# Kernel optimization log

Measured on AMD Instinct MI355X. Metric: run time of the kernel, lower is better.

The kernel has to match this reference:

```python
import jax, jax.numpy as jnp
import numpy as np

BS, NA, NE_, NL = 128, 3, 3, 3
NALL = NA - 1                 # n_allies
ENT = NA + NE_ + NL           # 9 entities
EM1 = ENT - 1                 # 8
HID = 64                      # hidden_dim
HEAD = 4
HIN = 9                       # hyper input dim
HYP = 64                      # hyper hidden dim
NRBF, RUB = 3, 10.0
EPS = 1e-7


def _lin_init(k, fan_in, fan_out):
    k1, k2 = jax.random.split(k)
    lim = 1.0 / np.sqrt(fan_in)
    w = jax.random.uniform(k1, (fan_in, fan_out), minval=-lim, maxval=lim, dtype=jnp.float32)
    b = jax.random.uniform(k2, (fan_out,), minval=-lim, maxval=lim, dtype=jnp.float32)
    return w, b


def setup_inputs():
    key = jax.random.key(0)
    ks = jax.random.split(key, 12)
    d = {}
    obs_dim = 4 + 2 * (NL + NALL + NE_) + 2 * (NALL + NE_)  # 30
    d["inputs"] = jax.random.normal(ks[0], (BS * NA, obs_dim), dtype=jnp.float32)
    d["hidden_state"] = jnp.zeros((1, HID), dtype=jnp.float32)
    d["actions"] = jax.random.normal(ks[1], (BS * NA, 2), dtype=jnp.float32)
    out_dim = (HIN + 1) * HID * HEAD  # 2560
    d["hA1_w"], d["hA1_b"] = _lin_init(ks[2], HIN, HYP)
    d["hA2_w"], d["hA2_b"] = _lin_init(ks[3], HYP, out_dim)
    d["hE1_w"], d["hE1_b"] = _lin_init(ks[4], HIN, HYP)
    d["hE2_w"], d["hE2_b"] = _lin_init(ks[5], HYP, out_dim)
    d["hL1_w"], d["hL1_b"] = _lin_init(ks[6], HIN, HYP)
    d["hL2_w"], d["hL2_b"] = _lin_init(ks[7], HYP, out_dim)
    d["merger_w"] = jnp.ones((1, HEAD, HID), dtype=jnp.float32)
    d["fc1_w"], d["fc1_b"] = _lin_init(ks[8], HID + 3, HID)
    d["fc2_w"], d["fc2_b"] = _lin_init(ks[9], HID, 1)
    return d


def _pair_out(feat, w1, b1, w2, b2):
    # hypernetwork: Linear(9,64) -> LeakyReLU -> Linear(64, (9+1)*64*4)
    h = jax.nn.leaky_relu(feat @ w1 + b1, negative_slope=0.01)
    out = h @ w2 + b2                               # (bs,NA,EM1,EM1,2560)
    nw = HIN * HID * HEAD
    w = out[..., :nw].reshape(feat.shape[:-1] + (HIN, HID * HEAD))
    b = out[..., nw:]
    y = jnp.einsum('...k,...kd->...d', feat, w) + b  # tiny 1x9 @ 9x256 per pair
    return y.reshape(feat.shape[:-1] + (HEAD, HID))


def _forward(inputs, actions, hA1_w, hA1_b, hA2_w, hA2_b, hE1_w, hE1_b, hE2_w, hE2_b,
             hL1_w, hL1_b, hL2_w, hL2_b, merger_w, fc1_w, fc1_b, fc2_w, fc2_b):
    bs = inputs.shape[0] // NA
    ob = inputs
    own = ob[:, :4].reshape(bs, NA, 4)
    i = 4
    lm_pos = ob[:, i:i + NL * 2].reshape(bs, NA, NL, 2); i += NL * 2
    ally_pos = ob[:, i:i + NALL * 2].reshape(bs, NA, NALL, 2); i += NALL * 2
    enemy_pos = ob[:, i:i + NE_ * 2].reshape(bs, NA, NE_, 2); i += NE_ * 2
    entity_pos = jnp.concatenate([ally_pos, enemy_pos, lm_pos], axis=-2)  # (bs,NA,EM1,2)
    ally_vel = ob[:, i:i + NALL * 2].reshape(bs, NA, NALL, 2); i += NALL * 2
    enemy_vel = ob[:, i:i + NE_ * 2].reshape(bs, NA, NE_, 2)
    lm_vel = jnp.zeros_like(lm_pos) - own[:, :, None, :2]
    entity_vel = jnp.concatenate([ally_vel, enemy_vel, lm_vel], axis=-2)  # (bs,NA,EM1,2)
    # rel_vel[b,a,j,i] = vel[i] - vel[j]
    rel_vel = entity_vel[:, :, None, :, :] - entity_vel[:, :, :, None, :]
    vel_norm = jnp.sqrt((entity_vel ** 2).sum(-1))
    sin_a = entity_vel[..., 1] / (vel_norm + EPS)
    cos_a = entity_vel[..., 0] / (vel_norm + EPS)
    act = actions.reshape(bs, NA, 2)
    act_norm = jnp.sqrt((act ** 2).sum(-1))        # (bs,NA)
    sin_b = act[..., 1] / (act_norm + EPS)
    cos_b = act[..., 0] / (act_norm + EPS)
    dist = jnp.sqrt((entity_pos ** 2).sum(-1))     # (bs,NA,EM1)
    sin_t = entity_pos[..., 1] / (dist + EPS)
    cos_t = entity_pos[..., 0] / (dist + EPS)
    # pair angles: A,C vary over last axis (i), B over second-to-last (j)
    sA, cA = sin_t[:, :, None, :], cos_t[:, :, None, :]
    sB, cB = sin_t[:, :, :, None], cos_t[:, :, :, None]
    sC, cC = sin_a[:, :, None, :], cos_a[:, :, None, :]
    angle_info = jnp.stack([sA * cB - cA * sB, cA * cB + sA * sB,
                            sC * cB - cC * sB, cC * cB + sC * sB], axis=-1)
    angle_info = jnp.broadcast_to(angle_info, (bs, NA, EM1, EM1, 4))
    sD, cD = sin_b[:, :, None], cos_b[:, :, None]
    act_angle = jnp.stack([sD * cos_t - cD * sin_t, cD * cos_t + sD * sin_t], axis=-1)  # (bs,NA,EM1,2)
    # gaussian RBF (schnet-style smearing, num_rbf=3, rbound_upper=10)
    offset = jnp.linspace(0.0, RUB, NRBF)
    coeff = -0.5 / (offset[1] - offset[0]) ** 2
    rbf = jnp.exp(coeff * (dist[..., None] - offset) ** 2)  # (bs,NA,EM1,NRBF)
    feat_dist = jnp.broadcast_to(rbf[:, :, None, :, :], (bs, NA, EM1, EM1, NRBF))
    feat = jnp.concatenate([feat_dist, angle_info, rel_vel], axis=-1)  # (bs,NA,EM1,EM1,9)
    ally_out = _pair_out(feat, hA1_w, hA1_b, hA2_w, hA2_b)
    enemy_out = _pair_out(feat, hE1_w, hE1_b, hE2_w, hE2_b)
    lm_out = _pair_out(feat, hL1_w, hL1_b, hL2_w, hL2_b)
    # type-based selection over the source-entity axis (dim 3), then sum-aggregate
    m = jnp.concatenate([ally_out[:, :, :, :NALL],
                         enemy_out[:, :, :, NALL:NALL + NE_],
                         lm_out[:, :, :, NALL + NE_:]], axis=3)
    m_sum = m.sum(axis=3)                               # (bs,NA,EM1,HEAD,HID)
    mw = jax.nn.softmax(merger_w, axis=1)               # (1,HEAD,HID)
    m_jki = (mw * m_sum).sum(axis=-2)                   # (bs,NA,EM1,HID)
    an = jnp.broadcast_to(act_norm[:, :, None], (bs, NA, EM1))[..., None]
    final = jnp.concatenate([m_jki, an, act_angle], axis=-1)  # (bs,NA,EM1,HID+3)
    x = jax.nn.relu(final)
    x = jax.nn.relu(x @ fc1_w + fc1_b)
    q = (x @ fc2_w + fc2_b).mean(axis=-2).reshape(-1, 1)  # (bs*NA,1)
    return q, x


def reference(inputs, hidden_state, actions, hA1_w, hA1_b, hA2_w, hA2_b,
              hE1_w, hE1_b, hE2_w, hE2_b, hL1_w, hL1_b, hL2_w, hL2_b,
              merger_w, fc1_w, fc1_b, fc2_w, fc2_b):
    q, x = _forward(inputs, actions, hA1_w, hA1_b, hA2_w, hA2_b,
                    hE1_w, hE1_b, hE2_w, hE2_b, hL1_w, hL1_b, hL2_w, hL2_b,
                    merger_w, fc1_w, fc1_b, fc2_w, fc2_b)
    return q, x
```

## Files before the change

### kernel.cpp

```cpp
#include <hip/hip_runtime.h>
#include <math.h>

#define EPS 1e-7f
#define ROWP 656
#define NETS 3
#define NROW_TOT (NETS*ROWP)
#define G4 (ROWP/4)
#define PERNET (ROWP*64)
#define PERNET4 (G4*64)

__global__ __launch_bounds__(256) void prep_w2r(
    const float* __restrict__ W2A, const float* __restrict__ b2A,
    const float* __restrict__ W2E, const float* __restrict__ b2E,
    const float* __restrict__ W2L, const float* __restrict__ b2L,
    const float* __restrict__ merger, float* __restrict__ W2r)
{
    int idx = blockIdx.x * 256 + threadIdx.x;
    if (idx >= NETS * PERNET4) return;
    int net = idx / PERNET4;
    int rem = idx - net * PERNET4;
    int g4  = rem >> 6;
    int hid = rem & 63;

    float m0 = merger[hid], m1 = merger[64+hid], m2 = merger[128+hid], m3 = merger[192+hid];
    float mx = fmaxf(fmaxf(m0, m1), fmaxf(m2, m3));
    float e0 = expf(m0-mx), e1 = expf(m1-mx), e2 = expf(m2-mx), e3 = expf(m3-mx);
    float inv = 1.0f / (e0+e1+e2+e3);
    float w0 = e0*inv, w1 = e1*inv, w2 = e2*inv, w3 = e3*inv;

    const float* W2 = (net==0) ? W2A : ((net==1) ? W2E : W2L);
    const float* b2 = (net==0) ? b2A : ((net==1) ? b2E : b2L);

    float4 v;
    float* vp = &v.x;
    #pragma unroll
    for (int r = 0; r < 4; ++r) {
        int row = g4*4 + r;
        float val = 0.0f;
        if (row < 650) {
            const float* src;
            int kk;
            if (row < 640) { int h = row / 10; kk = row - h*10; src = W2 + h*2560; }
            else           { kk = row - 640;                    src = b2; }
            int col = (kk < 9) ? kk*256 : 2304;
            val = w0*src[col+hid] + w1*src[col+64+hid] + w2*src[col+128+hid] + w3*src[col+192+hid];
        }
        vp[r] = val;
    }
    ((float4*)W2r)[idx] = v;
}

__global__ __launch_bounds__(256) void agent_kernel(
    const float* __restrict__ inputs, const float* __restrict__ actions,
    const float* __restrict__ W1A, const float* __restrict__ b1A,
    const float* __restrict__ W1E, const float* __restrict__ b1E,
    const float* __restrict__ W1L, const float* __restrict__ b1L,
    const float* __restrict__ W2r,
    const float* __restrict__ fc1w, const float* __restrict__ fc1b,
    const float* __restrict__ fc2w, const float* __restrict__ fc2b,
    float* __restrict__ out_q, float* __restrict__ out_x)
{
    __shared__ float sOb[32];
    __shared__ float sSt[8], sCt[8], sSa[8], sCa[8], sVx[8], sVy[8];
    __shared__ float sRbf[8][3];
    __shared__ float sAct[3];
    __shared__ float sF[64][10];
    __shared__ __align__(16) float sU[8 * NROW_TOT];
    __shared__ float sZp[4][8][64];
    __shared__ float sZ[8][64];
    __shared__ float sRed[4];

    const int tid   = threadIdx.x;
    const int agent = blockIdx.x;

    if (tid < 30) sOb[tid] = inputs[agent*30 + tid];
    if (tid == 30) sOb[30] = actions[agent*2 + 0];
    if (tid == 31) sOb[31] = actions[agent*2 + 1];
    __syncthreads();

    if (tid < 8) {
        int e = tid;
        float px, py, vx, vy;
        if (e < 2)      {           px = sOb[10+2*e]; py = sOb[11+2*e]; vx = sOb[20+2*e]; vy = sOb[21+2*e]; }
        else if (e < 5) { int t=e-2; px = sOb[14+2*t]; py = sOb[15+2*t]; vx = sOb[24+2*t]; vy = sOb[25+2*t]; }
        else            { int t=e-5; px = sOb[4+2*t];  py = sOb[5+2*t];  vx = -sOb[0];     vy = -sOb[1]; }
        float d  = sqrtf(px*px + py*py);
        sSt[e] = py / (d + EPS);
        sCt[e] = px / (d + EPS);
        float vn = sqrtf(vx*vx + vy*vy);
        sSa[e] = vy / (vn + EPS);
        sCa[e] = vx / (vn + EPS);
        sVx[e] = vx; sVy[e] = vy;
        sRbf[e][0] = expf(-0.02f * d * d);
        float d5  = d - 5.0f;  sRbf[e][1] = expf(-0.02f * d5  * d5);
        float d10 = d - 10.0f; sRbf[e][2] = expf(-0.02f * d10 * d10);
    }
    if (tid == 8) {
        float ax = sOb[30], ay = sOb[31];
        float an = sqrtf(ax*ax + ay*ay);
        sAct[0] = an;
        sAct[1] = ay / (an + EPS);
        sAct[2] = ax / (an + EPS);
    }
    __syncthreads();

    if (tid < 64) {
        int p = tid, j = p >> 3, k = p & 7;
        sF[p][0] = sRbf[k][0];
        sF[p][1] = sRbf[k][1];
        sF[p][2] = sRbf[k][2];
        sF[p][3] = sSt[k]*sCt[j] - sCt[k]*sSt[j];
        sF[p][4] = sCt[k]*sCt[j] + sSt[k]*sSt[j];
        sF[p][5] = sSa[k]*sCt[j] - sCa[k]*sSt[j];
        sF[p][6] = sCa[k]*sCt[j] + sSa[k]*sSt[j];
        sF[p][7] = sVx[k] - sVx[j];
        sF[p][8] = sVy[k] - sVy[j];
        sF[p][9] = 1.0f;
    }
    __syncthreads();

    for (int e = tid; e < 1920; e += 256) {
        if (e < 1536) {
            int j = e / 192, rem = e - j*192;
            int net = rem >> 6, h = rem & 63;
            int ks = (net==0) ? 0 : ((net==1) ? 2 : 5);
            int kn = (net==0) ? 2 : 3;
            const float* W1 = (net==0) ? W1A : ((net==1) ? W1E : W1L);
            const float* b1 = (net==0) ? b1A : ((net==1) ? b1E : b1L);
            float v[10];
            #pragma unroll
            for (int kk = 0; kk < 10; ++kk) v[kk] = 0.0f;
            for (int q = 0; q < kn; ++q) {
                int p = j*8 + ks + q;
                float acc = b1[h];
                #pragma unroll
                for (int kk = 0; kk < 9; ++kk) acc = fmaf(sF[p][kk], W1[kk*64 + h], acc);
                float H = (acc > 0.0f) ? acc : 0.01f*acc;
                #pragma unroll
                for (int kk = 0; kk < 10; ++kk) v[kk] = fmaf(H, sF[p][kk], v[kk]);
            }
            float* dst = sU + j*NROW_TOT + net*ROWP + h*10;
            #pragma unroll
            for (int kk = 0; kk < 10; ++kk) dst[kk] = v[kk];
        } else if (e < 1776) {
            int t = e - 1536;
            int j = t / 30, rem = t - j*30;
            int net = rem / 10, kk = rem - net*10;
            int ks = (net==0) ? 0 : ((net==1) ? 2 : 5);
            int kn = (net==0) ? 2 : 3;
            float v = 0.0f;
            for (int q = 0; q < kn; ++q) v += sF[j*8 + ks + q][kk];
            sU[j*NROW_TOT + net*ROWP + 640 + kk] = v;
        } else {
            int t = e - 1776;
            int j = t / 18, rem = t - j*18;
            int net = rem / 6, r = rem - net*6;
            sU[j*NROW_TOT + net*ROWP + 650 + r] = 0.0f;
        }
    }
    __syncthreads();

    {
        int lane = tid & 63, w = tid >> 6;
        float acc[8];
        #pragma unroll
        for (int j = 0; j < 8; ++j) acc[j] = 0.0f;
        const float4* Wp = (const float4*)W2r;
        for (int net = 0; net < NETS; ++net) {
            const float4* Wn = Wp + net*PERNET4;
            const float*  Ub = sU + net*ROWP;
            #pragma unroll 2
            for (int g = w; g < G4; g += 4) {
                float4 wv = Wn[g*64 + lane];
                int row = g*4;
                #pragma unroll
                for (int j = 0; j < 8; ++j) {
                    float4 u = *(const float4*)(Ub + j*NROW_TOT + row);
                    acc[j] = fmaf(u.x, wv.x, fmaf(u.y, wv.y, fmaf(u.z, wv.z, fmaf(u.w, wv.w, acc[j]))));
                }
            }
        }
        #pragma unroll
        for (int j = 0; j < 8; ++j) sZp[w][j][lane] = acc[j];
    }
    __syncthreads();
    for (int o = tid; o < 512; o += 256) {
        int j = o >> 6, c = o & 63;
        float z = sZp[0][j][c] + sZp[1][j][c] + sZp[2][j][c] + sZp[3][j][c];
        sZ[j][c] = (z > 0.0f) ? z : 0.0f;
    }
    __syncthreads();

    {
        float an  = sAct[0], sb = sAct[1], cb = sAct[2];
        float anr = (an > 0.0f) ? an : 0.0f;
        float myq = 0.0f;
        #pragma unroll
        for (int i = 0; i < 2; ++i) {
            int o = i*256 + tid;
            int j = o >> 6, c = o & 63;
            float acc = fc1b[c];
            #pragma unroll 8
            for (int d = 0; d < 64; ++d)
                acc = fmaf(sZ[j][d], fc1w[d*64 + c], acc);
            float aa0 = sb*sCt[j] - cb*sSt[j];
            float aa1 = cb*sCt[j] + sb*sSt[j];
            aa0 = (aa0 > 0.0f) ? aa0 : 0.0f;
            aa1 = (aa1 > 0.0f) ? aa1 : 0.0f;
            acc = fmaf(anr, fc1w[64*64 + c], acc);
            acc = fmaf(aa0, fc1w[65*64 + c], acc);
            acc = fmaf(aa1, fc1w[66*64 + c], acc);
            float x1 = (acc > 0.0f) ? acc : 0.0f;
            out_x[(agent*8 + j)*64 + c] = x1;
            myq = fmaf(x1, fc2w[c], myq);
        }
        for (int off = 32; off; off >>= 1) myq += __shfl_down(myq, off);
        int lane = tid & 63, w = tid >> 6;
        if (lane == 0) sRed[w] = myq;
        __syncthreads();
        if (tid == 0) out_q[agent] = (sRed[0] + sRed[1] + sRed[2] + sRed[3]) * 0.125f + fc2b[0];
    }
}

extern "C" void kernel_launch(void* const* d_in, const int* in_sizes, int n_in,
                              void* d_out, int out_size, void* d_ws, size_t ws_size,
                              hipStream_t stream) {
    const float* inputs  = (const float*)d_in[0];
    const float* actions = (const float*)d_in[2];
    const float* hA1_w = (const float*)d_in[3];  const float* hA1_b = (const float*)d_in[4];
    const float* hA2_w = (const float*)d_in[5];  const float* hA2_b = (const float*)d_in[6];
    const float* hE1_w = (const float*)d_in[7];  const float* hE1_b = (const float*)d_in[8];
    const float* hE2_w = (const float*)d_in[9];  const float* hE2_b = (const float*)d_in[10];
    const float* hL1_w = (const float*)d_in[11]; const float* hL1_b = (const float*)d_in[12];
    const float* hL2_w = (const float*)d_in[13]; const float* hL2_b = (const float*)d_in[14];
    const float* merger = (const float*)d_in[15];
    const float* fc1w = (const float*)d_in[16];  const float* fc1b = (const float*)d_in[17];
    const float* fc2w = (const float*)d_in[18];  const float* fc2b = (const float*)d_in[19];

    float* W2r = (float*)d_ws;
    float* q   = (float*)d_out;
    float* x   = q + 384;

    int total4 = NETS * PERNET4;
    prep_w2r<<<(total4 + 255)/256, 256, 0, stream>>>(hA2_w, hA2_b, hE2_w, hE2_b,
                                                     hL2_w, hL2_b, merger, W2r);
    agent_kernel<<<384, 256, 0, stream>>>(inputs, actions,
                                          hA1_w, hA1_b, hE1_w, hE1_b, hL1_w, hL1_b,
                                          W2r, fc1w, fc1b, fc2w, fc2b, q, x);
}
```

Measured before the change: 128.1 us.

## Reorder W2 rows k-major and register-tile the hyper GEMV over four hidden columns

The packed W2 rows are reordered to be k-major (row = kk*64 + h), and the sU staging is written to match. In the main reduction each lane now loads four weight float4s spanning 16-column strides and reuses each shared-memory U float4 across four outputs, with cross-quarter partial sums combined by xor shuffles. The aim is to cut LDS traffic per FMA and raise ILP, at the cost of more registers, which is why launch_bounds now requests a minimum of 2 blocks. A tail row-group is handled only by the q==0 lanes, and the 10-iteration split per wave assumes G4=164 divides into 4 waves of 41 groups.

```diff
diff --git a/kernel.cpp b/kernel.cpp
--- a/kernel.cpp
+++ b/kernel.cpp
@@ -6,7 +6,7 @@
 #define NETS 3
 #define NROW_TOT (NETS*ROWP)
 #define G4 (ROWP/4)
-#define PERNET (ROWP*64)
+#define GPW (G4/4)
 #define PERNET4 (G4*64)
 
 __global__ __launch_bounds__(256) void prep_w2r(
@@ -40,8 +40,8 @@
         if (row < 650) {
             const float* src;
             int kk;
-            if (row < 640) { int h = row / 10; kk = row - h*10; src = W2 + h*2560; }
-            else           { kk = row - 640;                    src = b2; }
+            if (row < 640) { kk = row >> 6; int h = row & 63; src = W2 + h*2560; }
+            else           { kk = row - 640;                  src = b2; }
             int col = (kk < 9) ? kk*256 : 2304;
             val = w0*src[col+hid] + w1*src[col+64+hid] + w2*src[col+128+hid] + w3*src[col+192+hid];
         }
@@ -50,7 +50,7 @@
     ((float4*)W2r)[idx] = v;
 }
 
-__global__ __launch_bounds__(256) void agent_kernel(
+__global__ __launch_bounds__(256, 2) void agent_kernel(
     const float* __restrict__ inputs, const float* __restrict__ actions,
     const float* __restrict__ W1A, const float* __restrict__ b1A,
     const float* __restrict__ W1E, const float* __restrict__ b1E,
@@ -139,9 +139,9 @@
                 #pragma unroll
                 for (int kk = 0; kk < 10; ++kk) v[kk] = fmaf(H, sF[p][kk], v[kk]);
             }
-            float* dst = sU + j*NROW_TOT + net*ROWP + h*10;
-            #pragma unroll
-            for (int kk = 0; kk < 10; ++kk) dst[kk] = v[kk];
+            float* dst = sU + j*NROW_TOT + net*ROWP + h;
+            #pragma unroll
+            for (int kk = 0; kk < 10; ++kk) dst[kk*64] = v[kk];
         } else if (e < 1776) {
             int t = e - 1536;
             int j = t / 30, rem = t - j*30;
@@ -161,27 +161,60 @@
     __syncthreads();
 
     {
-        int lane = tid & 63, w = tid >> 6;
-        float acc[8];
+        const int lane = tid & 63, w = tid >> 6;
+        const int q = lane >> 4, hh = lane & 15;
+        float acc[8][4];
         #pragma unroll
-        for (int j = 0; j < 8; ++j) acc[j] = 0.0f;
+        for (int j = 0; j < 8; ++j)
+            #pragma unroll
+            for (int k = 0; k < 4; ++k) acc[j][k] = 0.0f;
+
         const float4* Wp = (const float4*)W2r;
+        const int base = w * GPW;
         for (int net = 0; net < NETS; ++net) {
             const float4* Wn = Wp + net*PERNET4;
             const float*  Ub = sU + net*ROWP;
             #pragma unroll 2
-            for (int g = w; g < G4; g += 4) {
-                float4 wv = Wn[g*64 + lane];
-                int row = g*4;
+            for (int u = 0; u < 10; ++u) {
+                int g = base + u*4 + q;
+                const float4* wb = Wn + g*64 + hh;
+                float4 wk0 = wb[0], wk1 = wb[16], wk2 = wb[32], wk3 = wb[48];
+                float4 uj[8];
+                #pragma unroll
+                for (int j = 0; j < 8; ++j) uj[j] = *(const float4*)(Ub + j*NROW_TOT + g*4);
                 #pragma unroll
                 for (int j = 0; j < 8; ++j) {
-                    float4 u = *(const float4*)(Ub + j*NROW_TOT + row);
-                    acc[j] = fmaf(u.x, wv.x, fmaf(u.y, wv.y, fmaf(u.z, wv.z, fmaf(u.w, wv.w, acc[j]))));
+                    float4 uu = uj[j];
+                    acc[j][0] = fmaf(uu.x,wk0.x, fmaf(uu.y,wk0.y, fmaf(uu.z,wk0.z, fmaf(uu.w,wk0.w, acc[j][0]))));
+                    acc[j][1] = fmaf(uu.x,wk1.x, fmaf(uu.y,wk1.y, fmaf(uu.z,wk1.z, fmaf(uu.w,wk1.w, acc[j][1]))));
+                    acc[j][2] = fmaf(uu.x,wk2.x, fmaf(uu.y,wk2.y, fmaf(uu.z,wk2.z, fmaf(uu.w,wk2.w, acc[j][2]))));
+                    acc[j][3] = fmaf(uu.x,wk3.x, fmaf(uu.y,wk3.y, fmaf(uu.z,wk3.z, fmaf(uu.w,wk3.w, acc[j][3]))));
                 }
             }
+            if (q == 0) {
+                int g = base + 40;
+                const float4* wb = Wn + g*64 + hh;
+                float4 wk0 = wb[0], wk1 = wb[16], wk2 = wb[32], wk3 = wb[48];
+                #pragma unroll
+                for (int j = 0; j < 8; ++j) {
+                    float4 uu = *(const float4*)(Ub + j*NROW_TOT + g*4);
+                    acc[j][0] = fmaf(uu.x,wk0.x, fmaf(uu.y,wk0.y, fmaf(uu.z,wk0.z, fmaf(uu.w,wk0.w, acc[j][0]))));
+                    acc[j][1] = fmaf(uu.x,wk1.x, fmaf(uu.y,wk1.y, fmaf(uu.z,wk1.z, fmaf(uu.w,wk1.w, acc[j][1]))));
+                    acc[j][2] = fmaf(uu.x,wk2.x, fmaf(uu.y,wk2.y, fmaf(uu.z,wk2.z, fmaf(uu.w,wk2.w, acc[j][2]))));
+                    acc[j][3] = fmaf(uu.x,wk3.x, fmaf(uu.y,wk3.y, fmaf(uu.z,wk3.z, fmaf(uu.w,wk3.w, acc[j][3]))));
+                }
+            }
         }
         #pragma unroll
-        for (int j = 0; j < 8; ++j) sZp[w][j][lane] = acc[j];
+        for (int j = 0; j < 8; ++j) {
+            #pragma unroll
+            for (int k = 0; k < 4; ++k) {
+                float v = acc[j][k];
+                v += __shfl_xor(v, 16);
+                v += __shfl_xor(v, 32);
+                if (q == 0) sZp[w][j][k*16 + hh] = v;
+            }
+        }
     }
     __syncthreads();
     for (int o = tid; o < 512; o += 256) {
```

New measurement: 121.0 us. 5.5% less time.
